# Kernel optimization log

Hardware: AMD Instinct MI355X
Metric: run time of the kernel (lower is better)

## Reference

```python
import jax, jax.numpy as jnp
import numpy as np

B, S, HID = 1, 2048, 2048
H = 16
D_NOPE, D_ROPE, D_V = 128, 64, 128
Q_HEAD = D_NOPE + D_ROPE  # 192
QL, KVL = 1536, 512
EPS = 1e-6
SCALE = Q_HEAD ** -0.5


def rms_norm(x, w, eps=EPS):
    return x * jax.lax.rsqrt(jnp.mean(x * x, axis=-1, keepdims=True) + eps) * w


def rotate_half(x):
    h = x.shape[-1] // 2
    return jnp.concatenate([-x[..., h:], x[..., :h]], axis=-1)


def apply_rope(x, cos, sin):
    # DeepSeek de-interleave: view(..., d//2, 2).transpose(-1,-2).reshape == [even, odd]
    x = jnp.concatenate([x[..., 0::2], x[..., 1::2]], axis=-1)
    return x * cos + rotate_half(x) * sin


def setup_inputs() -> dict:
    key = jax.random.key(0)
    ks = jax.random.split(key, 8)
    x = jax.random.normal(ks[0], (B, S, HID), dtype=jnp.float32)
    # causal additive mask
    causal = jnp.tril(jnp.ones((S, S), dtype=bool))
    mask = jnp.where(causal, 0.0, -1e9).astype(jnp.float32)[None, None]
    position_ids = jnp.broadcast_to(jnp.arange(S, dtype=jnp.int32), (B, S))
    # RoPE caches, theta=10000
    inv_freq = 1.0 / (10000.0 ** (np.arange(0, D_ROPE, 2, dtype=np.float32) / D_ROPE))
    freqs = np.outer(np.arange(S, dtype=np.float32), inv_freq)
    emb = np.concatenate([freqs, freqs], axis=-1)
    cos = jnp.asarray(np.cos(emb), dtype=jnp.float32)
    sin = jnp.asarray(np.sin(emb), dtype=jnp.float32)
    w = lambda k, shp: (jax.random.normal(k, shp, dtype=jnp.float32) * 0.02)
    return {
        "x": x, "mask": mask, "position_ids": position_ids, "cos": cos, "sin": sin,
        "q_a_w": w(ks[1], (HID, QL)),
        "q_a_ln": jnp.ones((QL,), jnp.float32),
        "q_b_w": w(ks[2], (QL, H * Q_HEAD)),
        "kv_a_w": w(ks[3], (HID, KVL + D_ROPE)),
        "kv_a_ln": jnp.ones((KVL,), jnp.float32),
        "kv_b_w": w(ks[4], (KVL, H * (D_NOPE + D_V))),
        "o_w": w(ks[5], (H * D_V, HID)),
    }


def reference(x, mask, position_ids, cos, sin, q_a_w, q_a_ln, q_b_w, kv_a_w, kv_a_ln, kv_b_w, o_w):
    b, s, _ = x.shape
    # low-rank Q projection
    q = rms_norm(x @ q_a_w, q_a_ln) @ q_b_w            # [B,S,H*192]
    q = q.reshape(b, s, H, Q_HEAD).transpose(0, 2, 1, 3)  # [B,H,S,192]
    q_nope, q_pe = q[..., :D_NOPE], q[..., D_NOPE:]
    # compressed KV + decoupled rope key (MQA, shared across heads)
    ckv = x @ kv_a_w                                   # [B,S,512+64]
    c_norm = rms_norm(ckv[..., :KVL], kv_a_ln)         # [B,S,512]
    k_pe = ckv[..., KVL:][:, None]                     # [B,1,S,64]
    kv = (c_norm @ kv_b_w).reshape(b, s, H, D_NOPE + D_V).transpose(0, 2, 1, 3)
    k_nope, value = kv[..., :D_NOPE], kv[..., D_NOPE:]  # [B,H,S,128] each
    # rope
    cos_p = cos[position_ids][:, None]                 # [B,1,S,64]
    sin_p = sin[position_ids][:, None]
    q_pe = apply_rope(q_pe, cos_p, sin_p)
    k_pe = apply_rope(k_pe, cos_p, sin_p)
    query = jnp.concatenate([q_nope, q_pe], axis=-1)   # [B,H,S,192]
    key = jnp.concatenate([k_nope, jnp.broadcast_to(k_pe, (b, H, s, D_ROPE))], axis=-1)
    scores = jnp.einsum("bhsd,bhtd->bhst", query, key) * SCALE + mask
    attn = jax.nn.softmax(scores, axis=-1)
    out = jnp.einsum("bhst,bhtd->bhsd", attn, value)   # [B,H,S,128]
    out = out.transpose(0, 2, 1, 3).reshape(b, s, H * D_V) @ o_w
    kv_cache = jnp.concatenate([c_norm, k_pe[:, 0]], axis=-1)  # [B,S,576] latent cache
    return out, kv_cache
```

## Files before the change

kernel.cpp:

```cpp
#include <hip/hip_runtime.h>

typedef unsigned short u16;
typedef __bf16 bf16x8 __attribute__((ext_vector_type(8)));
typedef short s16x4 __attribute__((ext_vector_type(4)));
typedef short s16x8 __attribute__((ext_vector_type(8)));
typedef float f32x4 __attribute__((ext_vector_type(4)));

#define S_LEN 2048
#define NHEAD 16
#define QHEAD 192
#define EPS 1e-6f
#define ATTN_SCALE 0.07216878364870323f
#define QSCALE_LOG2E 0.10412011228586118f

__device__ __forceinline__ u16 f2bf(float f) {
    unsigned u = __builtin_bit_cast(unsigned, f);
    u = (u + 0x7FFFu + ((u >> 16) & 1u)) >> 16;
    return (u16)u;
}
__device__ __forceinline__ float bf2f(u16 h) {
    unsigned u = ((unsigned)h) << 16;
    return __builtin_bit_cast(float, u);
}

__device__ __forceinline__ void gl_lds16(const u16* g, u16* l) {
    __builtin_amdgcn_global_load_lds(
        (const __attribute__((address_space(1))) unsigned int*)g,
        (__attribute__((address_space(3))) unsigned int*)l,
        16, 0, 0);
}

#if defined(__has_builtin) && __has_builtin(__builtin_amdgcn_mfma_f32_16x16x16bf16_1k)
__device__ __forceinline__ f32x4 mfma16(s16x4 a, s16x4 b, f32x4 c) {
    return __builtin_amdgcn_mfma_f32_16x16x16bf16_1k(a, b, c, 0, 0, 0);
}
#else
__device__ __forceinline__ f32x4 mfma16(s16x4 a, s16x4 b, f32x4 c) {
    asm volatile("v_mfma_f32_16x16x16_bf16 %0, %1, %2, %0"
                 : "+v"(c) : "v"(a), "v"(b));
    return c;
}
#endif

template <int CF32>
__device__ __forceinline__ void gemm_core(
    u16* __restrict__ smem,
    const u16* __restrict__ A, const u16* __restrict__ B, void* __restrict__ Cv,
    int K, int lda, int ldb, int ldc, int tm, int tn)
{
    const int tid = threadIdx.x;
    const int w = tid >> 6, lane = tid & 63;
    const int q = lane >> 4, r = lane & 15;

    const int lr = lane & 15;
    const int lc = (lane >> 4) * 8;
    const u16* ga0 = A + (long)(tm * 128 + w * 32 + lr) * lda + lc;
    const u16* ga1 = ga0 + 16 * (long)lda;
    const u16* gb0 = B + (long)(tn * 128 + w * 32 + lr) * ldb + lc;
    const u16* gb1 = gb0 + 16 * (long)ldb;
    const int sa0 = w * 1024, sa1 = sa0 + 512;
    const int sb0 = 4096 + w * 1024, sb1 = sb0 + 512;

    f32x4 acc[4][4] = {};
    const int wm = w >> 1;
    const int wn = w & 1;
    const int n = K >> 5;

    gl_lds16(ga0, smem + sa0);
    gl_lds16(ga1, smem + sa1);
    gl_lds16(gb0, smem + sb0);
    gl_lds16(gb1, smem + sb1);
    gl_lds16(ga0 + 32, smem + 8192 + sa0);
    gl_lds16(ga1 + 32, smem + 8192 + sa1);
    gl_lds16(gb0 + 32, smem + 8192 + sb0);
    gl_lds16(gb1 + 32, smem + 8192 + sb1);
    asm volatile("s_waitcnt vmcnt(4)" ::: "memory");
    __builtin_amdgcn_sched_barrier(0);
    __builtin_amdgcn_s_barrier();
    __builtin_amdgcn_sched_barrier(0);

    int bc = 0;
    for (int t = 0; t < n; ++t) {
        u16* const cur = smem + bc * 8192;
        if (t + 2 < n) {
            int bn = bc + 2; if (bn >= 3) bn -= 3;
            u16* const nxt = smem + bn * 8192;
            const long k2 = (long)(t + 2) << 5;
            gl_lds16(ga0 + k2, nxt + sa0);
            gl_lds16(ga1 + k2, nxt + sa1);
            gl_lds16(gb0 + k2, nxt + sb0);
            gl_lds16(gb1 + k2, nxt + sb1);
        }
        bf16x8 af[4], bv[4];
        #pragma unroll
        for (int mt = 0; mt < 4; ++mt)
            af[mt] = *(const bf16x8*)&cur[(wm * 4 + mt) * 512 + lane * 8];
        #pragma unroll
        for (int nt = 0; nt < 4; ++nt)
            bv[nt] = *(const bf16x8*)&cur[4096 + (wn * 4 + nt) * 512 + lane * 8];
        #pragma unroll
        for (int mt = 0; mt < 4; ++mt)
            #pragma unroll
            for (int nt = 0; nt < 4; ++nt)
                acc[mt][nt] = __builtin_amdgcn_mfma_f32_16x16x32_bf16(
                    af[mt], bv[nt], acc[mt][nt], 0, 0, 0);
        if (t + 1 < n) {
            if (t + 2 < n) asm volatile("s_waitcnt vmcnt(4)" ::: "memory");
            else           asm volatile("s_waitcnt vmcnt(0)" ::: "memory");
            __builtin_amdgcn_sched_barrier(0);
            __builtin_amdgcn_s_barrier();
            __builtin_amdgcn_sched_barrier(0);
        }
        if (++bc == 3) bc = 0;
    }

    const int row0 = tm * 128 + wm * 64 + q * 4;
    const int col0 = tn * 128 + wn * 64 + r;
    if (CF32) {
        float* C = (float*)Cv;
        #pragma unroll
        for (int mt = 0; mt < 4; ++mt)
            #pragma unroll
            for (int i = 0; i < 4; ++i) {
                long rb = (long)(row0 + mt * 16 + i) * ldc + col0;
                #pragma unroll
                for (int nt = 0; nt < 4; ++nt)
                    C[rb + nt * 16] = acc[mt][nt][i];
            }
    } else {
        u16* C = (u16*)Cv;
        #pragma unroll
        for (int mt = 0; mt < 4; ++mt)
            #pragma unroll
            for (int i = 0; i < 4; ++i) {
                long rb = (long)(row0 + mt * 16 + i) * ldc + col0;
                #pragma unroll
                for (int nt = 0; nt < 4; ++nt)
                    C[rb + nt * 16] = f2bf(acc[mt][nt][i]);
            }
    }
}

template <int CF32>
__global__ __launch_bounds__(256, 2)
void gemm_bt(const u16* __restrict__ A, const u16* __restrict__ B,
             void* __restrict__ Cv, int K, int lda, int ldb, int ldc)
{
    __shared__ __align__(16) u16 smem[3 * 8192];
    gemm_core<CF32>(smem, A, B, Cv, K, lda, ldb, ldc, blockIdx.y, blockIdx.x);
}

__global__ __launch_bounds__(256, 2)
void gemm_bt_dual(const u16* __restrict__ A0, const u16* __restrict__ B0,
                  void* __restrict__ C0, int K0, int lda0, int ldb0, int ldc0, int nx0,
                  const u16* __restrict__ A1, const u16* __restrict__ B1,
                  void* __restrict__ C1, int K1, int lda1, int ldb1, int ldc1, int nx1)
{
    __shared__ __align__(16) u16 smem[3 * 8192];
    if (blockIdx.z == 0) {
        if ((int)blockIdx.x >= nx0) return;
        gemm_core<0>(smem, A0, B0, C0, K0, lda0, ldb0, ldc0, blockIdx.y, blockIdx.x);
    } else {
        if ((int)blockIdx.x >= nx1) return;
        gemm_core<0>(smem, A1, B1, C1, K1, lda1, ldb1, ldc1, blockIdx.y, blockIdx.x);
    }
}

template<int C0, int C1>
__device__ __forceinline__ void stage_tile(
    const u16* __restrict__ kvb, const u16* __restrict__ kpe,
    const u16* __restrict__ vt,
    u16* __restrict__ Kl, u16* __restrict__ Vl,
    int h, int t, int quad, int r)
{
    #pragma unroll
    for (int c = C0; c < C1; ++c) {
        if (c < 24) {
            const int mtk = c / 6, kc = c % 6;
            const int row = t * 64 + mtk * 16 + r;
            const u16* src = (kc < 4)
                ? kvb + (size_t)row * 4096 + h * 256 + kc * 32 + quad * 8
                : kpe + (size_t)row * 64 + (kc - 4) * 32 + quad * 8;
            gl_lds16(src, &Kl[c * 512]);
        } else {
            const int cv = c - 24, mtd = cv >> 1, sc = cv & 1;
            const u16* src = vt + ((size_t)h * 128 + mtd * 16 + r) * 2048
                             + t * 64 + sc * 32 + quad * 8;
            gl_lds16(src, &Vl[cv * 512]);
        }
    }
}

__device__ __forceinline__ void stage_dispatch(
    const u16* __restrict__ kvb, const u16* __restrict__ kpe,
    const u16* __restrict__ vt,
    u16* __restrict__ Kl, u16* __restrict__ Vl,
    int w, int h, int t, int quad, int r)
{
    if (w == 0) stage_tile<0, 20>(kvb, kpe, vt, Kl, Vl, h, t, quad, r);
    else        stage_tile<20, 40>(kvb, kpe, vt, Kl, Vl, h, t, quad, r);
}

__device__ __forceinline__ void kv_tile_step(
    const u16* __restrict__ Kl, const u16* __restrict__ Vl,
    const bf16x8 (&Qf)[2][6], f32x4 (&Oacc)[8][2], float (&lsum)[2],
    int lane, int quad, int r, int kglob0, int qg0, int qg1, bool maskT)
{
    f32x4 Sacc[4][2];
    #pragma unroll
    for (int mtk = 0; mtk < 4; ++mtk) {
        Sacc[mtk][0] = (f32x4){0.f, 0.f, 0.f, 0.f};
        Sacc[mtk][1] = (f32x4){0.f, 0.f, 0.f, 0.f};
    }
    #pragma unroll
    for (int kc = 0; kc < 6; ++kc)
        #pragma unroll
        for (int mtk = 0; mtk < 4; ++mtk) {
            bf16x8 Ak = *(const bf16x8*)&Kl[(mtk * 6 + kc) * 512 + lane * 8];
            Sacc[mtk][0] = __builtin_amdgcn_mfma_f32_16x16x32_bf16(
                Ak, Qf[0][kc], Sacc[mtk][0], 0, 0, 0);
            Sacc[mtk][1] = __builtin_amdgcn_mfma_f32_16x16x32_bf16(
                Ak, Qf[1][kc], Sacc[mtk][1], 0, 0, 0);
        }
    #pragma unroll
    for (int sc = 0; sc < 2; ++sc) {
        s16x4 Pf[2][2];
        #pragma unroll
        for (int nn = 0; nn < 2; ++nn) {
            const int qg = nn ? qg1 : qg0;
            #pragma unroll
            for (int half = 0; half < 2; ++half) {
                const int kb = sc * 2 + half;
                const int kb0 = kglob0 + kb * 16 + quad * 4;
                #pragma unroll
                for (int i = 0; i < 4; ++i) {
                    float pv = exp2f(Sacc[kb][nn][i]);
                    if (maskT && (kb0 + i > qg)) pv = 0.f;
                    lsum[nn] += pv;
                    Pf[nn][half][i] = (short)f2bf(pv);
                }
            }
        }
        #pragma unroll
        for (int mtd = 0; mtd < 8; ++mtd) {
            s16x8 Av8 = *(const s16x8*)&Vl[(mtd * 2 + sc) * 512 + quad * 128 + r * 8];
            s16x4 lo = __builtin_shufflevector(Av8, Av8, 0, 1, 2, 3);
            s16x4 hi = __builtin_shufflevector(Av8, Av8, 4, 5, 6, 7);
            Oacc[mtd][0] = mfma16(lo, Pf[0][0], Oacc[mtd][0]);
            Oacc[mtd][0] = mfma16(hi, Pf[0][1], Oacc[mtd][0]);
            Oacc[mtd][1] = mfma16(lo, Pf[1][0], Oacc[mtd][1]);
            Oacc[mtd][1] = mfma16(hi, Pf[1][1], Oacc[mtd][1]);
        }
    }
}

__global__ __launch_bounds__(128, 1)
void flash_attn(const u16* __restrict__ query, const u16* __restrict__ kvb,
                const u16* __restrict__ kpe, const u16* __restrict__ vt,
                u16* __restrict__ ao)
{
    const int tid = threadIdx.x;
    const int w = tid >> 6, lane = tid & 63;
    const int quad = lane >> 4, r = lane & 15;

    const int bid = (int)blockIdx.x;
    const int i = bid & 255;
    const int t_ = i >> 4;
    const int h = i & 15;
    const int j = (bid < 256) ? (31 - t_) : t_;

    const int q0 = j * 64;
    const int ntk = j + 1;

    __shared__ __align__(16) u16 smem[40960];

    const int qg0 = q0 + w * 32 + r;
    const int qg1 = qg0 + 16;

    bf16x8 Qf[2][6];
    #pragma unroll
    for (int nn = 0; nn < 2; ++nn)
        #pragma unroll
        for (int kc = 0; kc < 6; ++kc)
            Qf[nn][kc] = *(const bf16x8*)(query
                + ((size_t)h * S_LEN + q0 + w * 32 + nn * 16 + r) * QHEAD
                + kc * 32 + quad * 8);

    f32x4 Oacc[8][2];
    #pragma unroll
    for (int mtd = 0; mtd < 8; ++mtd) {
        Oacc[mtd][0] = (f32x4){0.f, 0.f, 0.f, 0.f};
        Oacc[mtd][1] = (f32x4){0.f, 0.f, 0.f, 0.f};
    }
    float lsum[2] = {0.f, 0.f};

    stage_dispatch(kvb, kpe, vt, smem, smem + 12288, w, h, 0, quad, r);
    __syncthreads();

    for (int t = 0; t < ntk; ++t) {
        u16* const curb = smem + (t & 1) * 20480;
        u16* const nxtb = smem + ((t + 1) & 1) * 20480;
        if (t + 1 < ntk)
            stage_dispatch(kvb, kpe, vt, nxtb, nxtb + 12288, w, h, t + 1, quad, r);
        kv_tile_step(curb, curb + 12288, Qf, Oacc, lsum,
                     lane, quad, r, t * 64, qg0, qg1, t == ntk - 1);
        __syncthreads();
    }

    #pragma unroll
    for (int nn = 0; nn < 2; ++nn) {
        float l = lsum[nn];
        l += __shfl_xor(l, 16, 64);
        l += __shfl_xor(l, 32, 64);
        const float inv = 1.0f / l;
        const int qrow = q0 + w * 32 + nn * 16 + r;
        #pragma unroll
        for (int mtd = 0; mtd < 8; ++mtd) {
            ushort4 o;
            o.x = f2bf(Oacc[mtd][nn][0] * inv);
            o.y = f2bf(Oacc[mtd][nn][1] * inv);
            o.z = f2bf(Oacc[mtd][nn][2] * inv);
            o.w = f2bf(Oacc[mtd][nn][3] * inv);
            *(ushort4*)(ao + (size_t)qrow * 2048 + h * 128 + mtd * 16 + quad * 4) = o;
        }
    }
}

__device__ __forceinline__ void wtrans_body(
    float (*tile)[33], const float* __restrict__ in, u16* __restrict__ out,
    int K, int N, int bx, int by, int tid)
{
    const int tx = tid & 31, ty = tid >> 5;
    const int k0 = bx * 32, n0 = by * 32;
    #pragma unroll
    for (int jj = 0; jj < 32; jj += 8) {
        int nn = n0 + tx;
        tile[ty + jj][tx] = (nn < N) ? in[(long)(k0 + ty + jj) * N + nn] : 0.0f;
    }
    __syncthreads();
    #pragma unroll
    for (int jj = 0; jj < 32; jj += 8)
        out[(long)(n0 + ty + jj) * K + k0 + tx] = f2bf(tile[tx][ty + jj]);
}

__global__ __launch_bounds__(256)
void prep_k(const float4* __restrict__ x4, ushort4* __restrict__ xb4,
            const float* __restrict__ q_a_w, const float* __restrict__ kv_a_w,
            const float* __restrict__ q_b_w, const float* __restrict__ kv_b_w,
            const float* __restrict__ o_w,
            u16* __restrict__ W1, u16* __restrict__ qbwt,
            u16* __restrict__ kvbwt, u16* __restrict__ owt)
{
    __shared__ float tile[32][33];
    const int tid = threadIdx.x;
    int b = (int)blockIdx.x;
    if (b < 4096) {
        int i = b * 256 + tid;
        float4 v = x4[i];
        ushort4 o;
        o.x = f2bf(v.x); o.y = f2bf(v.y); o.z = f2bf(v.z); o.w = f2bf(v.w);
        xb4[i] = o;
        return;
    }
    b -= 4096;
    if (b < 3072)       wtrans_body(tile, q_a_w,  W1,                  2048, 1536, b % 64, b / 64, tid);
    else if ((b -= 3072) < 1280) wtrans_body(tile, kv_a_w, W1 + 1536ULL * 2048, 2048, 576,  b % 64, b / 64, tid);
    else if ((b -= 1280) < 4608) wtrans_body(tile, q_b_w,  qbwt,       1536, 3072, b % 48, b / 48, tid);
    else if ((b -= 4608) < 2048) wtrans_body(tile, kv_b_w, kvbwt,      512,  4096, b % 16, b / 16, tid);
    else { b -= 2048;            wtrans_body(tile, o_w,    owt,        2048, 2048, b % 64, b / 64, tid); }
}

__global__ __launch_bounds__(256)
void norm_k(u16* __restrict__ qkv, const float* __restrict__ q_ln,
            const float* __restrict__ kv_ln, const int* __restrict__ pos_ids,
            const float* __restrict__ cosb, const float* __restrict__ sinb,
            float* __restrict__ kvout, u16* __restrict__ cnb,
            u16* __restrict__ kpe)
{
    const int s = blockIdx.x, tid = threadIdx.x;
    u16* row = qkv + (long)s * 2176;
    u16* row2 = row + 1536;
    __shared__ float red[8];
    float sum = 0.f;
    for (int d = tid; d < 1536; d += 256) { float v = bf2f(row[d]); sum += v * v; }
    #pragma unroll
    for (int o = 32; o; o >>= 1) sum += __shfl_xor(sum, o, 64);
    if ((tid & 63) == 0) red[tid >> 6] = sum;
    float sum2 = 0.f;
    for (int d = tid; d < 512; d += 256) { float v = bf2f(row2[d]); sum2 += v * v; }
    #pragma unroll
    for (int o = 32; o; o >>= 1) sum2 += __shfl_xor(sum2, o, 64);
    if ((tid & 63) == 0) red[4 + (tid >> 6)] = sum2;
    __syncthreads();
    sum  = red[0] + red[1] + red[2] + red[3];
    sum2 = red[4] + red[5] + red[6] + red[7];
    const float sc1 = rsqrtf(sum / 1536.f + EPS);
    const float sc2 = rsqrtf(sum2 / 512.f + EPS);
    for (int d = tid; d < 1536; d += 256)
        row[d] = f2bf(bf2f(row[d]) * sc1 * q_ln[d]);
    for (int d = tid; d < 512; d += 256) {
        float v = bf2f(row2[d]) * sc2 * kv_ln[d];
        kvout[(long)s * 576 + d] = v;
        cnb[(long)s * 512 + d] = f2bf(v);
    }
    if (tid < 32) {
        int p = pos_ids[s];
        float x0 = bf2f(row2[512 + 2 * tid]);
        float x1 = bf2f(row2[512 + 2 * tid + 1]);
        float c1 = cosb[p * 64 + tid], s1 = sinb[p * 64 + tid];
        float c2 = cosb[p * 64 + 32 + tid], s2 = sinb[p * 64 + 32 + tid];
        float lo = x0 * c1 - x1 * s1;
        float hi = x1 * c2 + x0 * s2;
        kvout[(long)s * 576 + 512 + tid] = lo;
        kvout[(long)s * 576 + 544 + tid] = hi;
        kpe[(long)s * 64 + tid] = f2bf(lo);
        kpe[(long)s * 64 + 32 + tid] = f2bf(hi);
    }
}

__global__ __launch_bounds__(256)
void post_k(const u16* __restrict__ qb, const int* __restrict__ pos_ids,
            const float* __restrict__ cosb, const float* __restrict__ sinb,
            u16* __restrict__ query, const u16* __restrict__ kv,
            u16* __restrict__ vt)
{
    __shared__ u16 tile[32][33];
    const int tid = threadIdx.x;
    int b = (int)blockIdx.x;
    if (b < 2048) {
        const int s = b;
        const u16* row = qb + (long)s * 3072;
        {
            int h = tid >> 4, c = tid & 15;
            const u16* src = &row[h * QHEAD + c * 8];
            u16* dst = &query[((long)(h * S_LEN + s)) * QHEAD + c * 8];
            ushort4 a = *(const ushort4*)src;
            ushort4 bb = *(const ushort4*)(src + 4);
            ushort4 oa, ob;
            oa.x = f2bf(bf2f(a.x) * QSCALE_LOG2E); oa.y = f2bf(bf2f(a.y) * QSCALE_LOG2E);
            oa.z = f2bf(bf2f(a.z) * QSCALE_LOG2E); oa.w = f2bf(bf2f(a.w) * QSCALE_LOG2E);
            ob.x = f2bf(bf2f(bb.x) * QSCALE_LOG2E); ob.y = f2bf(bf2f(bb.y) * QSCALE_LOG2E);
            ob.z = f2bf(bf2f(bb.z) * QSCALE_LOG2E); ob.w = f2bf(bf2f(bb.w) * QSCALE_LOG2E);
            *(ushort4*)dst = oa;
            *(ushort4*)(dst + 4) = ob;
        }
        int p = pos_ids[s];
        for (int idx = tid; idx < 512; idx += 256) {
            int h = idx >> 5, i = idx & 31;
            float x0 = bf2f(row[h * QHEAD + 128 + 2 * i]);
            float x1 = bf2f(row[h * QHEAD + 128 + 2 * i + 1]);
            float c1 = cosb[p * 64 + i], s1 = sinb[p * 64 + i];
            float c2 = cosb[p * 64 + 32 + i], s2 = sinb[p * 64 + 32 + i];
            u16* qr = query + ((long)(h * S_LEN + s)) * QHEAD;
            qr[128 + i] = f2bf((x0 * c1 - x1 * s1) * QSCALE_LOG2E);
            qr[160 + i] = f2bf((x1 * c2 + x0 * s2) * QSCALE_LOG2E);
        }
    } else {
        b -= 2048;
        const int s0 = (b & 63) * 32, d0 = ((b >> 6) & 3) * 32, h = b >> 8;
        const int tx = tid & 31, ty = tid >> 5;
        #pragma unroll
        for (int jj = 0; jj < 32; jj += 8)
            tile[ty + jj][tx] = kv[(long)(s0 + ty + jj) * 4096 + h * 256 + 128 + d0 + tx];
        __syncthreads();
        const int txp = ((tx >> 2) & 3) * 8 + (tx >> 4) * 4 + (tx & 3);
        #pragma unroll
        for (int jj = 0; jj < 32; jj += 8)
            vt[(long)(h * 128 + d0 + ty + jj) * S_LEN + s0 + txp] = tile[tx][ty + jj];
    }
}

extern "C" void kernel_launch(void* const* d_in, const int* in_sizes, int n_in,
                              void* d_out, int out_size, void* d_ws, size_t ws_size,
                              hipStream_t stream)
{
    const float* x      = (const float*)d_in[0];
    const int*   posid  = (const int*)d_in[2];
    const float* cosb   = (const float*)d_in[3];
    const float* sinb   = (const float*)d_in[4];
    const float* q_a_w  = (const float*)d_in[5];
    const float* q_a_ln = (const float*)d_in[6];
    const float* q_b_w  = (const float*)d_in[7];
    const float* kv_a_w = (const float*)d_in[8];
    const float* kv_a_ln= (const float*)d_in[9];
    const float* kv_b_w = (const float*)d_in[10];
    const float* o_w    = (const float*)d_in[11];

    float* out    = (float*)d_out;
    float* kv_out = out + (size_t)2048 * 2048;

    char* ws = (char*)d_ws;
    size_t off = 0;
    auto alloc = [&](size_t bytes) { char* p = ws + off; off += (bytes + 255) & ~(size_t)255; return p; };
    u16* xb    = (u16*)alloc(2048ULL * 2048 * 2);
    u16* W1    = (u16*)alloc(2176ULL * 2048 * 2);
    u16* qbwt  = (u16*)alloc(3072ULL * 1536 * 2);
    u16* kvbwt = (u16*)alloc(4096ULL * 512 * 2);
    u16* owt   = (u16*)alloc(2048ULL * 2048 * 2);
    u16* qkv_a = (u16*)alloc(2048ULL * 2176 * 2);
    u16* qbuf  = (u16*)alloc(2048ULL * 3072 * 2);
    u16* query = (u16*)alloc(16ULL * 2048 * 192 * 2);
    u16* cnb   = (u16*)alloc(2048ULL * 512 * 2);
    u16* kpe   = (u16*)alloc(2048ULL * 64 * 2);
    u16* kvbuf = (u16*)alloc(2048ULL * 4096 * 2);
    u16* vt    = (u16*)alloc(16ULL * 128 * 2048 * 2);
    u16* ao    = (u16*)alloc(2048ULL * 2048 * 2);
    (void)ws_size; (void)in_sizes; (void)n_in; (void)out_size;

    dim3 blk(256);

    prep_k<<<dim3(19200), blk, 0, stream>>>(
        (const float4*)x, (ushort4*)xb, q_a_w, kv_a_w, q_b_w, kv_b_w, o_w,
        W1, qbwt, kvbwt, owt);

    gemm_bt<0><<<dim3(17, 16), blk, 0, stream>>>(xb, W1, qkv_a, 2048, 2048, 2048, 2176);

    norm_k<<<dim3(2048), blk, 0, stream>>>(qkv_a, q_a_ln, kv_a_ln, posid,
                                           cosb, sinb, kv_out, cnb, kpe);

    gemm_bt_dual<<<dim3(32, 16, 2), blk, 0, stream>>>(
        qkv_a, qbwt, qbuf, 1536, 2176, 1536, 3072, 24,
        cnb, kvbwt, kvbuf, 512, 512, 512, 4096, 32);

    post_k<<<dim3(6144), blk, 0, stream>>>(qbuf, posid, cosb, sinb, query, kvbuf, vt);

    flash_attn<<<dim3(512), dim3(128), 0, stream>>>(query, kvbuf, kpe, vt, ao);

    gemm_bt<1><<<dim3(16, 16), blk, 0, stream>>>(ao, owt, out, 2048, 2048, 2048, 2048);
}
```

Measured before the change: 427.7 us.

## Use K=64 double-buffered GEMM steps and four-wave flash attention blocks

The GEMM main loop moves from a triple-buffered K=32 pipeline to a double-buffered K=64 pipeline, halving the number of barriers per K and doing two MFMA sub-steps per stage, but it now waits for all loads (vmcnt(0)) before each barrier. Flash attention goes from 2 waves with 32 query rows each to 4 waves with 16 rows each. This halves per-thread accumulator registers, raises occupancy via launch_bounds(256,2) and spreads the K/V staging over four waves. The trade-offs are less load/compute overlap in the GEMM and each K/V tile being read from LDS by more waves per query row.

```diff
diff --git a/kernel.cpp b/kernel.cpp
--- a/kernel.cpp
+++ b/kernel.cpp
@@ -64,7 +64,7 @@
     f32x4 acc[4][4] = {};
     const int wm = w >> 1;
     const int wn = w & 1;
-    const int n = K >> 5;
+    const int n = K >> 6;
 
     gl_lds16(ga0, smem + sa0);
     gl_lds16(ga1, smem + sa1);
@@ -74,44 +74,48 @@
     gl_lds16(ga1 + 32, smem + 8192 + sa1);
     gl_lds16(gb0 + 32, smem + 8192 + sb0);
     gl_lds16(gb1 + 32, smem + 8192 + sb1);
-    asm volatile("s_waitcnt vmcnt(4)" ::: "memory");
+    asm volatile("s_waitcnt vmcnt(0)" ::: "memory");
     __builtin_amdgcn_sched_barrier(0);
     __builtin_amdgcn_s_barrier();
     __builtin_amdgcn_sched_barrier(0);
 
-    int bc = 0;
     for (int t = 0; t < n; ++t) {
-        u16* const cur = smem + bc * 8192;
-        if (t + 2 < n) {
-            int bn = bc + 2; if (bn >= 3) bn -= 3;
-            u16* const nxt = smem + bn * 8192;
-            const long k2 = (long)(t + 2) << 5;
-            gl_lds16(ga0 + k2, nxt + sa0);
-            gl_lds16(ga1 + k2, nxt + sa1);
-            gl_lds16(gb0 + k2, nxt + sb0);
-            gl_lds16(gb1 + k2, nxt + sb1);
-        }
-        bf16x8 af[4], bv[4];
-        #pragma unroll
-        for (int mt = 0; mt < 4; ++mt)
-            af[mt] = *(const bf16x8*)&cur[(wm * 4 + mt) * 512 + lane * 8];
-        #pragma unroll
-        for (int nt = 0; nt < 4; ++nt)
-            bv[nt] = *(const bf16x8*)&cur[4096 + (wn * 4 + nt) * 512 + lane * 8];
-        #pragma unroll
-        for (int mt = 0; mt < 4; ++mt)
+        u16* const cur = smem + (t & 1) * 16384;
+        u16* const nxt = smem + ((t + 1) & 1) * 16384;
+        if (t + 1 < n) {
+            const long k1 = (long)(t + 1) << 6;
+            gl_lds16(ga0 + k1, nxt + sa0);
+            gl_lds16(ga1 + k1, nxt + sa1);
+            gl_lds16(gb0 + k1, nxt + sb0);
+            gl_lds16(gb1 + k1, nxt + sb1);
+            gl_lds16(ga0 + k1 + 32, nxt + 8192 + sa0);
+            gl_lds16(ga1 + k1 + 32, nxt + 8192 + sa1);
+            gl_lds16(gb0 + k1 + 32, nxt + 8192 + sb0);
+            gl_lds16(gb1 + k1 + 32, nxt + 8192 + sb1);
+        }
+        #pragma unroll
+        for (int kk = 0; kk < 2; ++kk) {
+            u16* const sub = cur + kk * 8192;
+            bf16x8 af[4], bv[4];
+            #pragma unroll
+            for (int mt = 0; mt < 4; ++mt)
+                af[mt] = *(const bf16x8*)&sub[(wm * 4 + mt) * 512 + lane * 8];
             #pragma unroll
             for (int nt = 0; nt < 4; ++nt)
-                acc[mt][nt] = __builtin_amdgcn_mfma_f32_16x16x32_bf16(
-                    af[mt], bv[nt], acc[mt][nt], 0, 0, 0);
+                bv[nt] = *(const bf16x8*)&sub[4096 + (wn * 4 + nt) * 512 + lane * 8];
+            #pragma unroll
+            for (int mt = 0; mt < 4; ++mt)
+                #pragma unroll
+                for (int nt = 0; nt < 4; ++nt)
+                    acc[mt][nt] = __builtin_amdgcn_mfma_f32_16x16x32_bf16(
+                        af[mt], bv[nt], acc[mt][nt], 0, 0, 0);
+        }
         if (t + 1 < n) {
-            if (t + 2 < n) asm volatile("s_waitcnt vmcnt(4)" ::: "memory");
-            else           asm volatile("s_waitcnt vmcnt(0)" ::: "memory");
+            asm volatile("s_waitcnt vmcnt(0)" ::: "memory");
             __builtin_amdgcn_sched_barrier(0);
             __builtin_amdgcn_s_barrier();
             __builtin_amdgcn_sched_barrier(0);
         }
-        if (++bc == 3) bc = 0;
     }
 
     const int row0 = tm * 128 + wm * 64 + q * 4;
@@ -146,7 +150,7 @@
 void gemm_bt(const u16* __restrict__ A, const u16* __restrict__ B,
              void* __restrict__ Cv, int K, int lda, int ldb, int ldc)
 {
-    __shared__ __align__(16) u16 smem[3 * 8192];
+    __shared__ __align__(16) u16 smem[2 * 16384];
     gemm_core<CF32>(smem, A, B, Cv, K, lda, ldb, ldc, blockIdx.y, blockIdx.x);
 }
 
@@ -156,7 +160,7 @@
                   const u16* __restrict__ A1, const u16* __restrict__ B1,
                   void* __restrict__ C1, int K1, int lda1, int ldb1, int ldc1, int nx1)
 {
-    __shared__ __align__(16) u16 smem[3 * 8192];
+    __shared__ __align__(16) u16 smem[2 * 16384];
     if (blockIdx.z == 0) {
         if ((int)blockIdx.x >= nx0) return;
         gemm_core<0>(smem, A0, B0, C0, K0, lda0, ldb0, ldc0, blockIdx.y, blockIdx.x);
@@ -197,48 +201,42 @@
     u16* __restrict__ Kl, u16* __restrict__ Vl,
     int w, int h, int t, int quad, int r)
 {
-    if (w == 0) stage_tile<0, 20>(kvb, kpe, vt, Kl, Vl, h, t, quad, r);
-    else        stage_tile<20, 40>(kvb, kpe, vt, Kl, Vl, h, t, quad, r);
+    if (w == 0)      stage_tile<0, 10>(kvb, kpe, vt, Kl, Vl, h, t, quad, r);
+    else if (w == 1) stage_tile<10, 20>(kvb, kpe, vt, Kl, Vl, h, t, quad, r);
+    else if (w == 2) stage_tile<20, 30>(kvb, kpe, vt, Kl, Vl, h, t, quad, r);
+    else             stage_tile<30, 40>(kvb, kpe, vt, Kl, Vl, h, t, quad, r);
 }
 
 __device__ __forceinline__ void kv_tile_step(
     const u16* __restrict__ Kl, const u16* __restrict__ Vl,
-    const bf16x8 (&Qf)[2][6], f32x4 (&Oacc)[8][2], float (&lsum)[2],
-    int lane, int quad, int r, int kglob0, int qg0, int qg1, bool maskT)
-{
-    f32x4 Sacc[4][2];
-    #pragma unroll
-    for (int mtk = 0; mtk < 4; ++mtk) {
-        Sacc[mtk][0] = (f32x4){0.f, 0.f, 0.f, 0.f};
-        Sacc[mtk][1] = (f32x4){0.f, 0.f, 0.f, 0.f};
-    }
+    const bf16x8 (&Qf)[6], f32x4 (&Oacc)[8], float& lsum,
+    int lane, int quad, int r, int kglob0, int qg, bool maskT)
+{
+    f32x4 Sacc[4];
+    #pragma unroll
+    for (int mtk = 0; mtk < 4; ++mtk)
+        Sacc[mtk] = (f32x4){0.f, 0.f, 0.f, 0.f};
     #pragma unroll
     for (int kc = 0; kc < 6; ++kc)
         #pragma unroll
         for (int mtk = 0; mtk < 4; ++mtk) {
             bf16x8 Ak = *(const bf16x8*)&Kl[(mtk * 6 + kc) * 512 + lane * 8];
-            Sacc[mtk][0] = __builtin_amdgcn_mfma_f32_16x16x32_bf16(
-                Ak, Qf[0][kc], Sacc[mtk][0], 0, 0, 0);
-            Sacc[mtk][1] = __builtin_amdgcn_mfma_f32_16x16x32_bf16(
-                Ak, Qf[1][kc], Sacc[mtk][1], 0, 0, 0);
+            Sacc[mtk] = __builtin_amdgcn_mfma_f32_16x16x32_bf16(
+                Ak, Qf[kc], Sacc[mtk], 0, 0, 0);
         }
     #pragma unroll
     for (int sc = 0; sc < 2; ++sc) {
-        s16x4 Pf[2][2];
-        #pragma unroll
-        for (int nn = 0; nn < 2; ++nn) {
-            const int qg = nn ? qg1 : qg0;
+        s16x4 Pf[2];
+        #pragma unroll
+        for (int half = 0; half < 2; ++half) {
+            const int kb = sc * 2 + half;
+            const int kb0 = kglob0 + kb * 16 + quad * 4;
             #pragma unroll
-            for (int half = 0; half < 2; ++half) {
-                const int kb = sc * 2 + half;
-                const int kb0 = kglob0 + kb * 16 + quad * 4;
-                #pragma unroll
-                for (int i = 0; i < 4; ++i) {
-                    float pv = exp2f(Sacc[kb][nn][i]);
-                    if (maskT && (kb0 + i > qg)) pv = 0.f;
-                    lsum[nn] += pv;
-                    Pf[nn][half][i] = (short)f2bf(pv);
-                }
+            for (int i = 0; i < 4; ++i) {
+                float pv = exp2f(Sacc[kb][i]);
+                if (maskT && (kb0 + i > qg)) pv = 0.f;
+                lsum += pv;
+                Pf[half][i] = (short)f2bf(pv);
             }
         }
         #pragma unroll
@@ -246,15 +244,13 @@
             s16x8 Av8 = *(const s16x8*)&Vl[(mtd * 2 + sc) * 512 + quad * 128 + r * 8];
             s16x4 lo = __builtin_shufflevector(Av8, Av8, 0, 1, 2, 3);
             s16x4 hi = __builtin_shufflevector(Av8, Av8, 4, 5, 6, 7);
-            Oacc[mtd][0] = mfma16(lo, Pf[0][0], Oacc[mtd][0]);
-            Oacc[mtd][0] = mfma16(hi, Pf[0][1], Oacc[mtd][0]);
-            Oacc[mtd][1] = mfma16(lo, Pf[1][0], Oacc[mtd][1]);
-            Oacc[mtd][1] = mfma16(hi, Pf[1][1], Oacc[mtd][1]);
-        }
-    }
-}
-
-__global__ __launch_bounds__(128, 1)
+            Oacc[mtd] = mfma16(lo, Pf[0], Oacc[mtd]);
+            Oacc[mtd] = mfma16(hi, Pf[1], Oacc[mtd]);
+        }
+    }
+}
+
+__global__ __launch_bounds__(256, 2)
 void flash_attn(const u16* __restrict__ query, const u16* __restrict__ kvb,
                 const u16* __restrict__ kpe, const u16* __restrict__ vt,
                 u16* __restrict__ ao)
@@ -274,25 +270,20 @@
 
     __shared__ __align__(16) u16 smem[40960];
 
-    const int qg0 = q0 + w * 32 + r;
-    const int qg1 = qg0 + 16;
-
-    bf16x8 Qf[2][6];
-    #pragma unroll
-    for (int nn = 0; nn < 2; ++nn)
-        #pragma unroll
-        for (int kc = 0; kc < 6; ++kc)
-            Qf[nn][kc] = *(const bf16x8*)(query
-                + ((size_t)h * S_LEN + q0 + w * 32 + nn * 16 + r) * QHEAD
-                + kc * 32 + quad * 8);
-
-    f32x4 Oacc[8][2];
-    #pragma unroll
-    for (int mtd = 0; mtd < 8; ++mtd) {
-        Oacc[mtd][0] = (f32x4){0.f, 0.f, 0.f, 0.f};
-        Oacc[mtd][1] = (f32x4){0.f, 0.f, 0.f, 0.f};
-    }
-    float lsum[2] = {0.f, 0.f};
+    const int qg = q0 + w * 16 + r;
+
+    bf16x8 Qf[6];
+    #pragma unroll
+    for (int kc = 0; kc < 6; ++kc)
+        Qf[kc] = *(const bf16x8*)(query
+            + ((size_t)h * S_LEN + q0 + w * 16 + r) * QHEAD
+            + kc * 32 + quad * 8);
+
+    f32x4 Oacc[8];
+    #pragma unroll
+    for (int mtd = 0; mtd < 8; ++mtd)
+        Oacc[mtd] = (f32x4){0.f, 0.f, 0.f, 0.f};
+    float lsum = 0.f;
 
     stage_dispatch(kvb, kpe, vt, smem, smem + 12288, w, h, 0, quad, r);
     __syncthreads();
@@ -303,26 +294,23 @@
         if (t + 1 < ntk)
             stage_dispatch(kvb, kpe, vt, nxtb, nxtb + 12288, w, h, t + 1, quad, r);
         kv_tile_step(curb, curb + 12288, Qf, Oacc, lsum,
-                     lane, quad, r, t * 64, qg0, qg1, t == ntk - 1);
+                     lane, quad, r, t * 64, qg, t == ntk - 1);
         __syncthreads();
     }
 
-    #pragma unroll
-    for (int nn = 0; nn < 2; ++nn) {
-        float l = lsum[nn];
-        l += __shfl_xor(l, 16, 64);
-        l += __shfl_xor(l, 32, 64);
-        const float inv = 1.0f / l;
-        const int qrow = q0 + w * 32 + nn * 16 + r;
-        #pragma unroll
-        for (int mtd = 0; mtd < 8; ++mtd) {
-            ushort4 o;
-            o.x = f2bf(Oacc[mtd][nn][0] * inv);
-            o.y = f2bf(Oacc[mtd][nn][1] * inv);
-            o.z = f2bf(Oacc[mtd][nn][2] * inv);
-            o.w = f2bf(Oacc[mtd][nn][3] * inv);
-            *(ushort4*)(ao + (size_t)qrow * 2048 + h * 128 + mtd * 16 + quad * 4) = o;
-        }
+    float l = lsum;
+    l += __shfl_xor(l, 16, 64);
+    l += __shfl_xor(l, 32, 64);
+    const float inv = 1.0f / l;
+    const int qrow = q0 + w * 16 + r;
+    #pragma unroll
+    for (int mtd = 0; mtd < 8; ++mtd) {
+        ushort4 o;
+        o.x = f2bf(Oacc[mtd][0] * inv);
+        o.y = f2bf(Oacc[mtd][1] * inv);
+        o.z = f2bf(Oacc[mtd][2] * inv);
+        o.w = f2bf(Oacc[mtd][3] * inv);
+        *(ushort4*)(ao + (size_t)qrow * 2048 + h * 128 + mtd * 16 + quad * 4) = o;
     }
 }
 
@@ -524,7 +512,7 @@
 
     post_k<<<dim3(6144), blk, 0, stream>>>(qbuf, posid, cosb, sinb, query, kvbuf, vt);
 
-    flash_attn<<<dim3(512), dim3(128), 0, stream>>>(query, kvbuf, kpe, vt, ao);
+    flash_attn<<<dim3(512), dim3(256), 0, stream>>>(query, kvbuf, kpe, vt, ao);
 
     gemm_bt<1><<<dim3(16, 16), blk, 0, stream>>>(ao, owt, out, 2048, 2048, 2048, 2048);
 }
```

Result: faster. 395.3 us (-7.6%).
